# Performance work log

Measured on AMD Instinct MI355X. Metric: run time of the kernel, lower is better.

Reference implementation:

```python
import math
import jax, jax.numpy as jnp
import numpy as np

HEADS = 16


def setup_inputs() -> dict:
    key = jax.random.key(0)
    k1, k2, k3 = jax.random.split(key, 3)
    bs, n_ctx, width = 2, 2048, 1024
    x = jax.random.normal(k1, (bs, n_ctx, width), dtype=jnp.float32)
    # init_scale=0.25 style small init for stability
    W_qkv = jax.random.normal(k2, (width, 3 * width), dtype=jnp.float32) * (0.25 / math.sqrt(width))
    b_qkv = jnp.zeros((3 * width,), dtype=jnp.float32)
    W_proj = jax.random.normal(k3, (width, width), dtype=jnp.float32) * (0.25 / math.sqrt(width))
    b_proj = jnp.zeros((width,), dtype=jnp.float32)
    return {"x": x, "W_qkv": W_qkv, "b_qkv": b_qkv, "W_proj": W_proj, "b_proj": b_proj}


def reference(x, W_qkv, b_qkv, W_proj, b_proj):
    bs, n_ctx, width = x.shape
    qkv = x @ W_qkv + b_qkv                     # [b, s, 3*width]
    attn_ch = width // HEADS                    # head dim
    qkv = qkv.reshape(bs, n_ctx, HEADS, 3 * attn_ch)
    q, k, v = jnp.split(qkv, 3, axis=-1)        # each [b, s, h, c]
    scale = 1.0 / math.sqrt(math.sqrt(attn_ch)) # applied to both q and k
    weight = jnp.einsum('bthc,bshc->bhts', q * scale, k * scale)
    weight = jax.nn.softmax(weight.astype(jnp.float32), axis=-1).astype(qkv.dtype)
    out = jnp.einsum('bhts,bshc->bthc', weight, v).reshape(bs, n_ctx, width)
    return out @ W_proj + b_proj
```

## Files before the change

kernel.cpp:

```cpp
#include <hip/hip_runtime.h>


using u16 = unsigned short;
typedef __attribute__((ext_vector_type(8))) short s16x8;
typedef __attribute__((ext_vector_type(4))) float f32x4;
typedef __attribute__((ext_vector_type(16))) float f32x16;

__device__ __forceinline__ u16 f2bf(float f) {
    unsigned x = __builtin_bit_cast(unsigned, f);
    x += 0x7fffu + ((x >> 16) & 1u);
    return (u16)(x >> 16);
}
__device__ __forceinline__ float bf2f(u16 u) {
    return __builtin_bit_cast(float, ((unsigned)u) << 16);
}
__device__ __forceinline__ unsigned pk2bf(float lo, float hi) {
    unsigned a = __builtin_bit_cast(unsigned, lo);
    unsigned b = __builtin_bit_cast(unsigned, hi);
    a += 0x7fffu + ((a >> 16) & 1u);
    b += 0x7fffu + ((b >> 16) & 1u);
    return (a >> 16) | (b & 0xffff0000u);
}
__device__ __forceinline__ void gll16(const void* g, void* l) {
    __builtin_amdgcn_global_load_lds(
        (const __attribute__((address_space(1))) unsigned int*)g,
        (__attribute__((address_space(3))) unsigned int*)l, 16, 0, 0);
}

#define MFMA(a, b, c)   __builtin_amdgcn_mfma_f32_16x16x32_bf16((a), (b), (c), 0, 0, 0)
#define MFMA32(a, b, c) __builtin_amdgcn_mfma_f32_32x32x16_bf16((a), (b), (c), 0, 0, 0)


__global__ __launch_bounds__(256) void convert_split(const float* __restrict__ in,
                                                     u16* __restrict__ H, u16* __restrict__ L, int n) {
    int i = (blockIdx.x * 256 + threadIdx.x) * 4;
    if (i >= n) return;
    float4 v = *(const float4*)(in + i);
    u16 h0 = f2bf(v.x), h1 = f2bf(v.y), h2 = f2bf(v.z), h3 = f2bf(v.w);
    ushort4 hh = { h0, h1, h2, h3 };
    ushort4 ll = { f2bf(v.x - bf2f(h0)), f2bf(v.y - bf2f(h1)), f2bf(v.z - bf2f(h2)), f2bf(v.w - bf2f(h3)) };
    *(ushort4*)(H + i) = hh;
    *(ushort4*)(L + i) = ll;
}

__global__ __launch_bounds__(256) void transpose_split(const float* __restrict__ W,
                                                       u16* __restrict__ TH, u16* __restrict__ TL,
                                                       int K, int N) {
    __shared__ float st[32][33];
    int n0 = blockIdx.x * 32, k0 = blockIdx.y * 32;
    int c = threadIdx.x & 31, r8 = threadIdx.x >> 5;
#pragma unroll
    for (int i = 0; i < 4; ++i) {
        int r = r8 + i * 8;
        st[r][c] = W[(size_t)(k0 + r) * N + n0 + c];
    }
    __syncthreads();
#pragma unroll
    for (int i = 0; i < 4; ++i) {
        int r = r8 + i * 8;
        float v = st[c][r];
        u16 h = f2bf(v);
        TH[(size_t)(n0 + r) * K + k0 + c] = h;
        TL[(size_t)(n0 + r) * K + k0 + c] = f2bf(v - bf2f(h));
    }
}


template <int EPI>
__global__ __launch_bounds__(256, 2) void gemm_bf16x3(
    const u16* __restrict__ AH, const u16* __restrict__ AL,
    const u16* __restrict__ BTH, const u16* __restrict__ BTL,
    const float* __restrict__ bias,
    u16* __restrict__ Qs, u16* __restrict__ Kb, u16* __restrict__ Vp,
    float* __restrict__ Out) {
    const int K = 1024;
    __shared__ u16 sAh[128][40], sAl[128][40], sBh[128][40], sBl[128][40];

    int m0 = blockIdx.y * 128, n0 = blockIdx.x * 128;
    int tid = threadIdx.x, lane = tid & 63, wv = tid >> 6;
    int g = lane >> 4, c16 = lane & 15;
    int wm = wv >> 1, wn = wv & 1;

    f32x4 acc[4][4] = {};

    for (int kt = 0; kt < 32; ++kt) {
        int k0 = kt * 32;
        s16x8 ra[2], rla[2], rb[2], rlb[2];
#pragma unroll
        for (int i = 0; i < 2; ++i) {
            int cc = i * 256 + tid;
            int rr = cc >> 2, ko = (cc & 3) * 8;
            ra[i]  = *(const s16x8*)(AH  + (size_t)(m0 + rr) * K + k0 + ko);
            rla[i] = *(const s16x8*)(AL  + (size_t)(m0 + rr) * K + k0 + ko);
            rb[i]  = *(const s16x8*)(BTH + (size_t)(n0 + rr) * K + k0 + ko);
            rlb[i] = *(const s16x8*)(BTL + (size_t)(n0 + rr) * K + k0 + ko);
        }
        __syncthreads();
#pragma unroll
        for (int i = 0; i < 2; ++i) {
            int cc = i * 256 + tid;
            int rr = cc >> 2, ko = (cc & 3) * 8;
            *(s16x8*)&sAh[rr][ko] = ra[i];
            *(s16x8*)&sAl[rr][ko] = rla[i];
            *(s16x8*)&sBh[rr][ko] = rb[i];
            *(s16x8*)&sBl[rr][ko] = rlb[i];
        }
        __syncthreads();

        s16x8 ah[4], al[4], bh[4], bl[4];
#pragma unroll
        for (int mi = 0; mi < 4; ++mi) {
            ah[mi] = *(const s16x8*)&sAh[wm * 64 + mi * 16 + c16][g * 8];
            al[mi] = *(const s16x8*)&sAl[wm * 64 + mi * 16 + c16][g * 8];
        }
#pragma unroll
        for (int ni = 0; ni < 4; ++ni) {
            bh[ni] = *(const s16x8*)&sBh[wn * 64 + ni * 16 + c16][g * 8];
            bl[ni] = *(const s16x8*)&sBl[wn * 64 + ni * 16 + c16][g * 8];
        }
#pragma unroll
        for (int mi = 0; mi < 4; ++mi)
#pragma unroll
            for (int ni = 0; ni < 4; ++ni) {
                f32x4 c = acc[mi][ni];
                c = MFMA(ah[mi], bh[ni], c);
                c = MFMA(al[mi], bh[ni], c);
                c = MFMA(ah[mi], bl[ni], c);
                acc[mi][ni] = c;
            }
    }

#pragma unroll
    for (int ni = 0; ni < 4; ++ni) {
        int col = n0 + wn * 64 + ni * 16 + c16;
        float bs = bias[col];
        if (EPI == 0) {
            int h = col / 192;
            int rm = col - h * 192;
#pragma unroll
            for (int mi = 0; mi < 4; ++mi)
#pragma unroll
                for (int r = 0; r < 4; ++r) {
                    int row = m0 + wm * 64 + mi * 16 + 4 * g + r;
                    int b = row >> 11, s = row & 2047;
                    int bh16 = b * 16 + h;
                    float val = acc[mi][ni][r] + bs;
                    if (rm < 64)
                        Qs[(((size_t)bh16 * 2048 + s) << 6) + rm] = f2bf(val * 0.18033688011112042f);
                    else if (rm < 128)
                        Kb[(((size_t)bh16 * 2048 + s) << 6) + rm - 64] = f2bf(val);
                    else {
                        int d = rm - 128;
                        int kg = s >> 4, k16 = s & 15;
                        int mm = (k16 & 3) | (((k16 >> 3) & 1) << 2) | (((k16 >> 2) & 1) << 3);
                        Vp[(((size_t)bh16 * 128 + kg) * 64 + d) * 16 + mm] = f2bf(val);
                    }
                }
        } else {
#pragma unroll
            for (int mi = 0; mi < 4; ++mi)
#pragma unroll
                for (int r = 0; r < 4; ++r) {
                    int row = m0 + wm * 64 + mi * 16 + 4 * g + r;
                    Out[(size_t)row * 1024 + col] = acc[mi][ni][r] + bs;
                }
        }
    }
}

__global__ __launch_bounds__(256, 2) void attn_fwd(
    const u16* __restrict__ Qs, const u16* __restrict__ Kb, const u16* __restrict__ Vp,
    u16* __restrict__ OH, u16* __restrict__ OL) {
    __shared__ u16 sKV[2][16][512];

    int id = blockIdx.x;
    int xcd = id & 7, li = id >> 3;
    int bh = xcd * 4 + (li >> 4);
    int qblk = li & 15;
    int tid = threadIdx.x, w = tid >> 6, lane = tid & 63;
    int l31 = lane & 31, h = lane >> 5;
    int q0 = (qblk * 4 + w) * 32;

    size_t base = (size_t)bh * 2048 * 64;
    size_t vbase = (size_t)bh * 131072;

    const u16* qp = Qs + base + (size_t)(q0 + l31) * 64 + 8 * h;
    s16x8 qf[4];
#pragma unroll
    for (int c = 0; c < 4; ++c) qf[c] = *(const s16x8*)(qp + 16 * c);

    const int pk0 = 2 * w, pk1 = 2 * w + 1;
    const u16* gk0 = Kb + base + (size_t)((pk0 >> 2) * 32 + l31) * 64 + 16 * (pk0 & 3) + 8 * h;
    const u16* gk1 = Kb + base + (size_t)((pk1 >> 2) * 32 + l31) * 64 + 16 * (pk1 & 3) + 8 * h;
    const u16* gv0 = Vp + vbase + (size_t)pk0 * 512 + (size_t)l31 * 16 + 8 * h;
    const u16* gv1 = Vp + vbase + (size_t)pk1 * 512 + (size_t)l31 * 16 + 8 * h;

    auto stage = [&](int buf, int jj) {
        size_t ko = (size_t)jj * 4096;
        gll16(gk0 + ko, &sKV[buf][pk0][0]);
        gll16(gk1 + ko, &sKV[buf][pk1][0]);
        gll16(gv0 + ko, &sKV[buf][8 + pk0][0]);
        gll16(gv1 + ko, &sKV[buf][8 + pk1][0]);
    };

    f32x16 o0 = {}, o1 = {};
    float m = -1e30f, ls = 0.f;
    const int lo = lane * 8;

    stage(0, 0);

    for (int jj = 0; jj < 32; ++jj) {
        int cur = jj & 1;
        __syncthreads();
        if (jj < 31) stage(cur ^ 1, jj + 1);

        s16x8 kf[8], vf[8];
#pragma unroll
        for (int i = 0; i < 8; ++i) {
            kf[i] = *(const s16x8*)&sKV[cur][i][lo];
            vf[i] = *(const s16x8*)&sKV[cur][8 + i][lo];
        }

        f32x16 s0 = {}, s1 = {};
        __builtin_amdgcn_s_setprio(1);
        s0 = MFMA32(kf[0], qf[0], s0);
        s0 = MFMA32(kf[1], qf[1], s0);
        s0 = MFMA32(kf[2], qf[2], s0);
        s0 = MFMA32(kf[3], qf[3], s0);
        s1 = MFMA32(kf[4], qf[0], s1);
        s1 = MFMA32(kf[5], qf[1], s1);
        s1 = MFMA32(kf[6], qf[2], s1);
        s1 = MFMA32(kf[7], qf[3], s1);
        __builtin_amdgcn_s_setprio(0);

        float t0 = fmaxf(s0[0], s1[0]), t1 = fmaxf(s0[1], s1[1]);
        float t2 = fmaxf(s0[2], s1[2]), t3 = fmaxf(s0[3], s1[3]);
#pragma unroll
        for (int r = 4; r < 16; r += 4) {
            t0 = fmaxf(t0, fmaxf(s0[r], s1[r]));
            t1 = fmaxf(t1, fmaxf(s0[r + 1], s1[r + 1]));
            t2 = fmaxf(t2, fmaxf(s0[r + 2], s1[r + 2]));
            t3 = fmaxf(t3, fmaxf(s0[r + 3], s1[r + 3]));
        }
        float pmax = fmaxf(fmaxf(t0, t1), fmaxf(t2, t3));
        pmax = fmaxf(pmax, __shfl_xor(pmax, 32));

        if (!__all(pmax <= m + 8.f)) {
            float mn = fmaxf(m, pmax);
            float f = __builtin_amdgcn_exp2f(m - mn);
            m = mn;
            ls *= f;
#pragma unroll
            for (int r = 0; r < 16; ++r) {
                float fb = __shfl(f, (r & 3) + 8 * (r >> 2) + 4 * h);
                o0[r] *= fb;
                o1[r] *= fb;
            }
        }

        float a0 = 0.f, a1 = 0.f, a2 = 0.f, a3 = 0.f;
#pragma unroll
        for (int r = 0; r < 16; r += 4) {
            s0[r]     = __builtin_amdgcn_exp2f(s0[r] - m);     a0 += s0[r];
            s0[r + 1] = __builtin_amdgcn_exp2f(s0[r + 1] - m); a1 += s0[r + 1];
            s0[r + 2] = __builtin_amdgcn_exp2f(s0[r + 2] - m); a2 += s0[r + 2];
            s0[r + 3] = __builtin_amdgcn_exp2f(s0[r + 3] - m); a3 += s0[r + 3];
            s1[r]     = __builtin_amdgcn_exp2f(s1[r] - m);     a0 += s1[r];
            s1[r + 1] = __builtin_amdgcn_exp2f(s1[r + 1] - m); a1 += s1[r + 1];
            s1[r + 2] = __builtin_amdgcn_exp2f(s1[r + 2] - m); a2 += s1[r + 2];
            s1[r + 3] = __builtin_amdgcn_exp2f(s1[r + 3] - m); a3 += s1[r + 3];
        }
        float sm = (a0 + a1) + (a2 + a3);
        sm += __shfl_xor(sm, 32);
        ls += sm;

        union { s16x8 v8; unsigned u[4]; } p00, p01, p10, p11;
#pragma unroll
        for (int k = 0; k < 4; ++k) {
            p00.u[k] = pk2bf(s0[2 * k], s0[2 * k + 1]);
            p01.u[k] = pk2bf(s0[8 + 2 * k], s0[9 + 2 * k]);
            p10.u[k] = pk2bf(s1[2 * k], s1[2 * k + 1]);
            p11.u[k] = pk2bf(s1[8 + 2 * k], s1[9 + 2 * k]);
        }

        __builtin_amdgcn_s_setprio(1);
        o0 = MFMA32(p00.v8, vf[0], o0);
        o1 = MFMA32(p00.v8, vf[1], o1);
        o0 = MFMA32(p01.v8, vf[2], o0);
        o1 = MFMA32(p01.v8, vf[3], o1);
        o0 = MFMA32(p10.v8, vf[4], o0);
        o1 = MFMA32(p10.v8, vf[5], o1);
        o0 = MFMA32(p11.v8, vf[6], o0);
        o1 = MFMA32(p11.v8, vf[7], o1);
        __builtin_amdgcn_s_setprio(0);
    }

    int b = bh >> 4, hh = bh & 15;
    float inv = 1.0f / ls;
#pragma unroll
    for (int r = 0; r < 16; ++r) {
        int cr = (r & 3) + 8 * (r >> 2) + 4 * h;
        float fb = __shfl(inv, cr);
        int row = q0 + cr;
        size_t idx = ((size_t)(b * 2048 + row)) * 1024 + hh * 64 + l31;
        float v0 = o0[r] * fb, v1 = o1[r] * fb;
        u16 h0 = f2bf(v0);
        OH[idx] = h0;
        OL[idx] = f2bf(v0 - bf2f(h0));
        u16 h1 = f2bf(v1);
        OH[idx + 32] = h1;
        OL[idx + 32] = f2bf(v1 - bf2f(h1));
    }
}


extern "C" void kernel_launch(void* const* d_in, const int* in_sizes, int n_in,
                              void* d_out, int out_size, void* d_ws, size_t ws_size,
                              hipStream_t stream) {
    const float* x     = (const float*)d_in[0];
    const float* Wqkv  = (const float*)d_in[1];
    const float* bqkv  = (const float*)d_in[2];
    const float* Wproj = (const float*)d_in[3];
    const float* bproj = (const float*)d_in[4];
    float* out = (float*)d_out;

    char* w = (char*)d_ws;
    const size_t SZ_X  = (size_t)4096 * 1024 * 2;
    const size_t SZ_WQ = (size_t)3072 * 1024 * 2;
    const size_t SZ_WP = (size_t)1024 * 1024 * 2;
    u16* XH  = (u16*)w; w += SZ_X;
    u16* XL  = (u16*)w; w += SZ_X;
    u16* WQH = (u16*)w; w += SZ_WQ;
    u16* WQL = (u16*)w; w += SZ_WQ;
    u16* WPH = (u16*)w; w += SZ_WP;
    u16* WPL = (u16*)w; w += SZ_WP;
    u16* Q_s = (u16*)w; w += SZ_X;
    u16* K_b = (u16*)w; w += SZ_X;
    u16* V_p = (u16*)w; w += SZ_X;
    u16* OHp = (u16*)w; w += SZ_X;
    u16* OLp = (u16*)w; w += SZ_X;

    convert_split<<<4096, 256, 0, stream>>>(x, XH, XL, 4096 * 1024);
    transpose_split<<<dim3(96, 32), 256, 0, stream>>>(Wqkv, WQH, WQL, 1024, 3072);
    transpose_split<<<dim3(32, 32), 256, 0, stream>>>(Wproj, WPH, WPL, 1024, 1024);
    gemm_bf16x3<0><<<dim3(24, 32), 256, 0, stream>>>(XH, XL, WQH, WQL, bqkv, Q_s, K_b, V_p, nullptr);
    attn_fwd<<<512, 256, 0, stream>>>(Q_s, K_b, V_p, OHp, OLp);
    gemm_bf16x3<1><<<dim3(8, 32), 256, 0, stream>>>(OHp, OLp, WPH, WPL, bproj, nullptr, nullptr, nullptr, out);
}
```

Baseline: 194.2 us.

## Double-buffer GEMM tiles via direct global-to-LDS loads with XCD-aware block mapping

The bf16x3 GEMM stops staging tiles through registers and instead uses global_load_lds into a double-buffered, fragment-ordered shared-memory layout, so the next k-tile is prefetched while MFMAs run on the current one. This also removes one barrier per iteration. The grid becomes 1D, with block IDs remapped so each XCD handles a contiguous range of N-columns, aiming at better L2 reuse of B tiles. The packed layout drops the padding, which could bring LDS bank conflicts, and correctness depends on gll16's async completion being covered by the single barrier.

```diff
diff --git a/kernel.cpp b/kernel.cpp
--- a/kernel.cpp
+++ b/kernel.cpp
@@ -73,50 +73,53 @@
     const float* __restrict__ bias,
     u16* __restrict__ Qs, u16* __restrict__ Kb, u16* __restrict__ Vp,
     float* __restrict__ Out) {
-    const int K = 1024;
-    __shared__ u16 sAh[128][40], sAl[128][40], sBh[128][40], sBl[128][40];
-
-    int m0 = blockIdx.y * 128, n0 = blockIdx.x * 128;
+    __shared__ u16 sP[2][32][512];
+
+    int id = blockIdx.x;
+    int xcd = id & 7, local = id >> 3;
+    int nPerX = gridDim.x >> 8;
+    int nb = xcd * nPerX + (local >> 5);
+    int mb = local & 31;
+    int m0 = mb * 128, n0 = nb * 128;
+
     int tid = threadIdx.x, lane = tid & 63, wv = tid >> 6;
     int g = lane >> 4, c16 = lane & 15;
     int wm = wv >> 1, wn = wv & 1;
+    const int lo8 = lane * 8;
+
+    const u16* src[8];
+#pragma unroll
+    for (int i = 0; i < 8; ++i) {
+        int p = wv * 8 + i;
+        const u16* arr = (p < 8) ? AH : (p < 16) ? AL : (p < 24) ? BTH : BTL;
+        int row0 = ((p < 16) ? m0 : n0) + (p & 7) * 16;
+        src[i] = arr + (size_t)(row0 + c16) * 1024 + g * 8;
+    }
 
     f32x4 acc[4][4] = {};
 
+#pragma unroll
+    for (int i = 0; i < 8; ++i) gll16(src[i], &sP[0][wv * 8 + i][0]);
+
     for (int kt = 0; kt < 32; ++kt) {
-        int k0 = kt * 32;
-        s16x8 ra[2], rla[2], rb[2], rlb[2];
-#pragma unroll
-        for (int i = 0; i < 2; ++i) {
-            int cc = i * 256 + tid;
-            int rr = cc >> 2, ko = (cc & 3) * 8;
-            ra[i]  = *(const s16x8*)(AH  + (size_t)(m0 + rr) * K + k0 + ko);
-            rla[i] = *(const s16x8*)(AL  + (size_t)(m0 + rr) * K + k0 + ko);
-            rb[i]  = *(const s16x8*)(BTH + (size_t)(n0 + rr) * K + k0 + ko);
-            rlb[i] = *(const s16x8*)(BTL + (size_t)(n0 + rr) * K + k0 + ko);
-        }
+        int cur = kt & 1;
         __syncthreads();
-#pragma unroll
-        for (int i = 0; i < 2; ++i) {
-            int cc = i * 256 + tid;
-            int rr = cc >> 2, ko = (cc & 3) * 8;
-            *(s16x8*)&sAh[rr][ko] = ra[i];
-            *(s16x8*)&sAl[rr][ko] = rla[i];
-            *(s16x8*)&sBh[rr][ko] = rb[i];
-            *(s16x8*)&sBl[rr][ko] = rlb[i];
-        }
-        __syncthreads();
+        if (kt < 31) {
+            int ko = (kt + 1) * 32;
+#pragma unroll
+            for (int i = 0; i < 8; ++i) gll16(src[i] + ko, &sP[cur ^ 1][wv * 8 + i][0]);
+        }
 
         s16x8 ah[4], al[4], bh[4], bl[4];
 #pragma unroll
         for (int mi = 0; mi < 4; ++mi) {
-            ah[mi] = *(const s16x8*)&sAh[wm * 64 + mi * 16 + c16][g * 8];
-            al[mi] = *(const s16x8*)&sAl[wm * 64 + mi * 16 + c16][g * 8];
+            ah[mi] = *(const s16x8*)&sP[cur][wm * 4 + mi][lo8];
+            al[mi] = *(const s16x8*)&sP[cur][8 + wm * 4 + mi][lo8];
         }
 #pragma unroll
         for (int ni = 0; ni < 4; ++ni) {
-            bh[ni] = *(const s16x8*)&sBh[wn * 64 + ni * 16 + c16][g * 8];
-            bl[ni] = *(const s16x8*)&sBl[wn * 64 + ni * 16 + c16][g * 8];
+            bh[ni] = *(const s16x8*)&sP[cur][16 + wn * 4 + ni][lo8];
+            bl[ni] = *(const s16x8*)&sP[cur][24 + wn * 4 + ni][lo8];
         }
 #pragma unroll
         for (int mi = 0; mi < 4; ++mi)
@@ -343,7 +346,7 @@
     convert_split<<<4096, 256, 0, stream>>>(x, XH, XL, 4096 * 1024);
     transpose_split<<<dim3(96, 32), 256, 0, stream>>>(Wqkv, WQH, WQL, 1024, 3072);
     transpose_split<<<dim3(32, 32), 256, 0, stream>>>(Wproj, WPH, WPL, 1024, 1024);
-    gemm_bf16x3<0><<<dim3(24, 32), 256, 0, stream>>>(XH, XL, WQH, WQL, bqkv, Q_s, K_b, V_p, nullptr);
+    gemm_bf16x3<0><<<768, 256, 0, stream>>>(XH, XL, WQH, WQL, bqkv, Q_s, K_b, V_p, nullptr);
     attn_fwd<<<512, 256, 0, stream>>>(Q_s, K_b, V_p, OHp, OLp);
-    gemm_bf16x3<1><<<dim3(8, 32), 256, 0, stream>>>(OHp, OLp, WPH, WPL, bproj, nullptr, nullptr, nullptr, out);
-}
+    gemm_bf16x3<1><<<256, 256, 0, stream>>>(OHp, OLp, WPH, WPL, bproj, nullptr, nullptr, nullptr, out);
+}
```

Result: slower. 216.9 us (+11.7%).

## Rewrite QKV GEMM with 256x256 tiles and async global-to-LDS double buffering

Applied to the files above, without the earlier changes.

Replaces the 128x128 register-staged QKV GEMM with a 512-thread kernel that uses 256x256 tiles. It loads A/B hi/lo panels directly into LDS via global_load_lds with a two-stage double buffer and vmcnt-based waits, and raises MFMA wave priority during the compute phase. The larger tile raises arithmetic intensity and the async loads overlap memory with MFMA. The cost is only 192 blocks on a 256-CU device, so some CUs sit idle, plus heavier register and LDS use (128 KB of LDS per block). The projection GEMM keeps the old kernel, split out without the template.

```diff
diff --git a/kernel.cpp b/kernel.cpp
--- a/kernel.cpp
+++ b/kernel.cpp
@@ -65,14 +65,108 @@
     }
 }
 
-
-template <int EPI>
-__global__ __launch_bounds__(256, 2) void gemm_bf16x3(
+__global__ __launch_bounds__(512, 2) void gemm256_qkv(
     const u16* __restrict__ AH, const u16* __restrict__ AL,
     const u16* __restrict__ BTH, const u16* __restrict__ BTL,
     const float* __restrict__ bias,
-    u16* __restrict__ Qs, u16* __restrict__ Kb, u16* __restrict__ Vp,
-    float* __restrict__ Out) {
+    u16* __restrict__ Qs, u16* __restrict__ Kb, u16* __restrict__ Vp) {
+    __shared__ u16 sP[2][64][512];
+
+    int id = blockIdx.x;
+    int mb = id / 12, nb = id % 12;
+    int m0 = mb * 256, n0 = nb * 256;
+
+    int tid = threadIdx.x, lane = tid & 63, wv = tid >> 6;
+    int g = lane >> 4, c16 = lane & 15;
+    int wm = wv >> 2, wn = wv & 3;
+    const int lo8 = lane * 8;
+
+    const u16* src[8];
+#pragma unroll
+    for (int i = 0; i < 8; ++i) {
+        int p = wv * 8 + i;
+        int arr = p >> 4;
+        const u16* bse = arr == 0 ? AH : arr == 1 ? AL : arr == 2 ? BTH : BTL;
+        int row0 = (arr < 2 ? m0 : n0) + (p & 15) * 16;
+        src[i] = bse + (size_t)(row0 + c16) * 1024 + g * 8;
+    }
+
+    f32x4 acc[8][4] = {};
+
+#pragma unroll
+    for (int i = 0; i < 8; ++i) gll16(src[i], &sP[0][wv * 8 + i][0]);
+#pragma unroll
+    for (int i = 0; i < 8; ++i) gll16(src[i] + 32, &sP[1][wv * 8 + i][0]);
+
+    for (int kt = 0; kt < 32; ++kt) {
+        int cur = kt & 1;
+        if (kt < 31) asm volatile("s_waitcnt vmcnt(8)" ::: "memory");
+        else         asm volatile("s_waitcnt vmcnt(0)" ::: "memory");
+        __builtin_amdgcn_s_barrier();
+        __builtin_amdgcn_sched_barrier(0);
+
+        s16x8 bh[4], bl[4];
+#pragma unroll
+        for (int ni = 0; ni < 4; ++ni) {
+            bh[ni] = *(const s16x8*)&sP[cur][32 + wn * 4 + ni][lo8];
+            bl[ni] = *(const s16x8*)&sP[cur][48 + wn * 4 + ni][lo8];
+        }
+        __builtin_amdgcn_s_setprio(1);
+#pragma unroll
+        for (int mi = 0; mi < 8; ++mi) {
+            s16x8 ah = *(const s16x8*)&sP[cur][wm * 8 + mi][lo8];
+            s16x8 al = *(const s16x8*)&sP[cur][16 + wm * 8 + mi][lo8];
+#pragma unroll
+            for (int ni = 0; ni < 4; ++ni) {
+                f32x4 c = acc[mi][ni];
+                c = MFMA(ah, bh[ni], c);
+                c = MFMA(al, bh[ni], c);
+                c = MFMA(ah, bl[ni], c);
+                acc[mi][ni] = c;
+            }
+        }
+        __builtin_amdgcn_s_setprio(0);
+        __builtin_amdgcn_s_barrier();
+        __builtin_amdgcn_sched_barrier(0);
+        if (kt < 30) {
+            int ko = (kt + 2) * 32;
+#pragma unroll
+            for (int i = 0; i < 8; ++i) gll16(src[i] + ko, &sP[cur][wv * 8 + i][0]);
+        }
+    }
+
+#pragma unroll
+    for (int ni = 0; ni < 4; ++ni) {
+        int col = n0 + wn * 64 + ni * 16 + c16;
+        float bs = bias[col];
+        int h = col / 192;
+        int rm = col - h * 192;
+#pragma unroll
+        for (int mi = 0; mi < 8; ++mi)
+#pragma unroll
+            for (int r = 0; r < 4; ++r) {
+                int row = m0 + wm * 128 + mi * 16 + 4 * g + r;
+                int b = row >> 11, s = row & 2047;
+                int bh16 = b * 16 + h;
+                float val = acc[mi][ni][r] + bs;
+                if (rm < 64)
+                    Qs[(((size_t)bh16 * 2048 + s) << 6) + rm] = f2bf(val * 0.18033688011112042f);
+                else if (rm < 128)
+                    Kb[(((size_t)bh16 * 2048 + s) << 6) + rm - 64] = f2bf(val);
+                else {
+                    int d = rm - 128;
+                    int kg = s >> 4, k16 = s & 15;
+                    int mm = (k16 & 3) | (((k16 >> 3) & 1) << 2) | (((k16 >> 2) & 1) << 3);
+                    Vp[(((size_t)bh16 * 128 + kg) * 64 + d) * 16 + mm] = f2bf(val);
+                }
+            }
+    }
+}
+
+__global__ __launch_bounds__(256, 2) void gemm128_proj(
+    const u16* __restrict__ AH, const u16* __restrict__ AL,
+    const u16* __restrict__ BTH, const u16* __restrict__ BTL,
+    const float* __restrict__ bias, float* __restrict__ Out) {
     const int K = 1024;
     __shared__ u16 sAh[128][40], sAl[128][40], sBh[128][40], sBl[128][40];
 
@@ -134,37 +228,13 @@
     for (int ni = 0; ni < 4; ++ni) {
         int col = n0 + wn * 64 + ni * 16 + c16;
         float bs = bias[col];
-        if (EPI == 0) {
-            int h = col / 192;
-            int rm = col - h * 192;
-#pragma unroll
-            for (int mi = 0; mi < 4; ++mi)
-#pragma unroll
-                for (int r = 0; r < 4; ++r) {
-                    int row = m0 + wm * 64 + mi * 16 + 4 * g + r;
-                    int b = row >> 11, s = row & 2047;
-                    int bh16 = b * 16 + h;
-                    float val = acc[mi][ni][r] + bs;
-                    if (rm < 64)
-                        Qs[(((size_t)bh16 * 2048 + s) << 6) + rm] = f2bf(val * 0.18033688011112042f);
-                    else if (rm < 128)
-                        Kb[(((size_t)bh16 * 2048 + s) << 6) + rm - 64] = f2bf(val);
-                    else {
-                        int d = rm - 128;
-                        int kg = s >> 4, k16 = s & 15;
-                        int mm = (k16 & 3) | (((k16 >> 3) & 1) << 2) | (((k16 >> 2) & 1) << 3);
-                        Vp[(((size_t)bh16 * 128 + kg) * 64 + d) * 16 + mm] = f2bf(val);
-                    }
-                }
-        } else {
-#pragma unroll
-            for (int mi = 0; mi < 4; ++mi)
-#pragma unroll
-                for (int r = 0; r < 4; ++r) {
-                    int row = m0 + wm * 64 + mi * 16 + 4 * g + r;
-                    Out[(size_t)row * 1024 + col] = acc[mi][ni][r] + bs;
-                }
-        }
+#pragma unroll
+        for (int mi = 0; mi < 4; ++mi)
+#pragma unroll
+            for (int r = 0; r < 4; ++r) {
+                int row = m0 + wm * 64 + mi * 16 + 4 * g + r;
+                Out[(size_t)row * 1024 + col] = acc[mi][ni][r] + bs;
+            }
     }
 }
 
@@ -343,7 +413,7 @@
     convert_split<<<4096, 256, 0, stream>>>(x, XH, XL, 4096 * 1024);
     transpose_split<<<dim3(96, 32), 256, 0, stream>>>(Wqkv, WQH, WQL, 1024, 3072);
     transpose_split<<<dim3(32, 32), 256, 0, stream>>>(Wproj, WPH, WPL, 1024, 1024);
-    gemm_bf16x3<0><<<dim3(24, 32), 256, 0, stream>>>(XH, XL, WQH, WQL, bqkv, Q_s, K_b, V_p, nullptr);
+    gemm256_qkv<<<192, 512, 0, stream>>>(XH, XL, WQH, WQL, bqkv, Q_s, K_b, V_p);
     attn_fwd<<<512, 256, 0, stream>>>(Q_s, K_b, V_p, OHp, OLp);
-    gemm_bf16x3<1><<<dim3(8, 32), 256, 0, stream>>>(OHp, OLp, WPH, WPL, bproj, nullptr, nullptr, nullptr, out);
-}
+    gemm128_proj<<<dim3(8, 32), 256, 0, stream>>>(OHp, OLp, WPH, WPL, bproj, out);
+}
```

Result: slower. 218.1 us (+12.3%).
